# Performance work log

Measured on AMD Instinct MI355X. Metric: run time of the kernel, lower is better.

The kernel has to match this reference:

```python
import jax, jax.numpy as jnp
import numpy as np

# Dims (match init_kwargs / input_specs)
B, N, DIM, HEADS, DHEAD, CHUNK = 1, 2048, 1024, 8, 128, 64
HID = 4 * DHEAD            # MemoryMLP expansion_factor=4.0
DI = HEADS * DHEAD         # dim_inner
EPS = 1e-6
MAX_LR = 1.0               # default_step_transform_max_lr


def rmsnorm(x, w):
    return x * jax.lax.rsqrt(jnp.mean(jnp.square(x), -1, keepdims=True) + EPS) * w


def mem_forward(w0, w1, g, x):
    # ResidualNorm(MemoryMLP): y = RMSNorm(gelu(x@w0)@w1)*g + x
    h = jax.nn.gelu(x @ w0, approximate=False) @ w1
    return rmsnorm(h, g) + x


def setup_inputs() -> dict:
    key = jax.random.key(0)
    ks = jax.random.split(key, 12)
    s = lambda i, shape, sc: jax.random.normal(ks[i], shape, jnp.float32) * sc
    return dict(
        x=s(0, (B, N, DIM), 1.0),
        store_norm_w=jnp.ones((DIM,), jnp.float32),
        ret_norm_w=jnp.ones((DIM,), jnp.float32),
        Wq=s(1, (DIM, DI), DIM ** -0.5),
        Wk=s(2, (DIM, DI), DIM ** -0.5),
        Wv=s(3, (DIM, DI), DIM ** -0.5),
        W_step=s(4, (DIM, HEADS), DIM ** -0.5), b_step=jnp.zeros((HEADS,), jnp.float32),
        W_mom=s(5, (DIM, HEADS), DIM ** -0.5), b_mom=jnp.zeros((HEADS,), jnp.float32),
        W_decay=s(6, (DIM, HEADS), DIM ** -0.5), b_decay=jnp.zeros((HEADS,), jnp.float32),
        gate_W=s(7, (DIM, HEADS), DIM ** -0.5),
        combine_W=s(8, (DI, DIM), DI ** -0.5),
        mem_w0=s(9, (HEADS, DHEAD, HID), DHEAD ** -0.5),
        mem_w1=s(10, (HEADS, HID, DHEAD), HID ** -0.5),
        mem_g=jnp.ones((HEADS, DHEAD), jnp.float32),
    )


def reference(x, store_norm_w, ret_norm_w, Wq, Wk, Wv, W_step, b_step,
              W_mom, b_mom, W_decay, b_decay, gate_W, combine_W,
              mem_w0, mem_w1, mem_g):
    b, n, _ = x.shape
    nc = n // CHUNK
    BH = b * HEADS

    # ---- store path ----
    s = rmsnorm(x, store_norm_w)                                 # b n dim
    lr = jax.nn.sigmoid(s @ W_step + b_step) * MAX_LR            # b n h (per-token adaptive step)
    pooled = s.reshape(b, nc, CHUNK, DIM).mean(2)                # b nc dim (AveragePool chunk rep)
    mom = jax.nn.sigmoid(pooled @ W_mom + b_mom)                 # b nc h
    dec = jax.nn.sigmoid(pooled @ W_decay + b_decay)             # b nc h

    def to_chunks(t):  # b n (h d) -> (b h) nc c d
        return t.reshape(b, nc, CHUNK, HEADS, DHEAD).transpose(0, 3, 1, 2, 4).reshape(BH, nc, CHUNK, DHEAD)

    k = to_chunks(s @ Wk)
    v = to_chunks(s @ Wv)
    lr_c = lr.reshape(b, nc, CHUNK, HEADS).transpose(0, 3, 1, 2).reshape(BH, nc, CHUNK)
    mom_bh = mom.transpose(0, 2, 1).reshape(BH, nc)
    dec_bh = dec.transpose(0, 2, 1).reshape(BH, nc)

    # init fast weights per (b h)  (per_head_learned_parameters=True)
    w0 = jnp.broadcast_to(mem_w0[None], (b, HEADS, DHEAD, HID)).reshape(BH, DHEAD, HID)
    w1 = jnp.broadcast_to(mem_w1[None], (b, HEADS, HID, DHEAD)).reshape(BH, HID, DHEAD)
    g = jnp.broadcast_to(mem_g[None], (b, HEADS, DHEAD)).reshape(BH, DHEAD)

    def chunk_loss(w0_, w1_, g_, kc, vc, lrc):
        pred = mem_forward(w0_, w1_, g_, kc)                     # c d
        return jnp.sum(jnp.mean(jnp.square(pred - vc), -1) * lrc)

    grad_chunk = jax.grad(chunk_loss, argnums=(0, 1, 2))
    # vmap over chunks (same weights per chunk, per-sample grads), then over (b h)
    grads = jax.vmap(jax.vmap(grad_chunk, in_axes=(None, None, None, 0, 0, 0)))(w0, w1, g, k, v, lr_c)
    surprises = tuple(-gr for gr in grads)                       # each (BH, nc, ...)

    def combine(a, c):
        ga, xa = a
        gb, xb = c
        return (ga * gb, gb * xa + xb)

    def lin_scan(gates, xs):
        # y_i = gates_i * y_{i-1} + xs_i over chunk axis (axis=1)
        return jax.lax.associative_scan(combine, (gates, xs), axis=1)

    def expand(gates, ref):
        return gates.reshape(gates.shape + (1,) * (ref.ndim - 2))

    # momentum scan per parameter tensor
    updates = tuple(lin_scan(expand(mom_bh, su), su)[1] for su in surprises)

    # weight update scan: W_i = (1 - decay_i) * W_{i-1} + momentum_i, W_{-1} = init
    per_chunk_weights = []
    for upd, w_init in zip(updates, (w0, w1, g)):
        gates = expand(1.0 - dec_bh, upd)
        cumg, y = lin_scan(gates, upd)
        w_seq = y + cumg * w_init[:, None]                       # (BH, nc, ...)
        # retrieval at chunk i uses weights updated through chunk i-1
        per_chunk_weights.append(jnp.concatenate([w_init[:, None], w_seq[:, :-1]], axis=1))
    w0_c, w1_c, g_c = per_chunk_weights

    # ---- retrieve path ----
    r = rmsnorm(x, ret_norm_w)
    q = to_chunks(r @ Wq)                                        # (BH, nc, c, d)
    pred = jax.vmap(jax.vmap(mem_forward))(w0_c, w1_c, g_c, q)   # (BH, nc, c, d)
    out = pred.reshape(b, HEADS, n, DHEAD)                       # b h n d
    gate = jax.nn.sigmoid(r @ gate_W)                            # b n h (retrieve_gate, heads>1)
    out = out * gate.transpose(0, 2, 1)[..., None]
    out = out.transpose(0, 2, 1, 3).reshape(b, n, DI) @ combine_W
    return out
```

## Files before the change

### kernel.cpp

```cpp
#include <hip/hip_runtime.h>
#include <hip/hip_bf16.h>
#include <math.h>

#define NH   8
#define DHD  128
#define HIDN 512
#define CHK  64
#define NCH  32
#define MB   1048576ull

typedef unsigned short u16;
typedef unsigned int   u32;
typedef short s16x8 __attribute__((ext_vector_type(8)));
typedef float f32x4 __attribute__((ext_vector_type(4)));

#define MFMA(a,b,c) __builtin_amdgcn_mfma_f32_16x16x32_bf16((a),(b),(c),0,0,0)

__device__ __forceinline__ float bf2f(u16 v){ return __uint_as_float(((u32)v) << 16); }
__device__ __forceinline__ u16 f2bf(float f){
  u32 u = __float_as_uint(f);
  u += 0x7fffu + ((u >> 16) & 1u);
  return (u16)(u >> 16);
}
__device__ __forceinline__ u32 pack2(float a, float b){
  return (u32)f2bf(a) | ((u32)f2bf(b) << 16);
}
__device__ __forceinline__ float dot2(u32 a, u32 b){
  return __uint_as_float(a << 16)*__uint_as_float(b << 16)
       + __uint_as_float(a & 0xffff0000u)*__uint_as_float(b & 0xffff0000u);
}
__device__ __forceinline__ float waveRedSum(float v){
  #pragma unroll
  for (int off = 32; off; off >>= 1) v += __shfl_xor(v, off);
  return v;
}
__device__ __forceinline__ void gload16(const void* g, void* l){
  __builtin_amdgcn_global_load_lds(
      (const __attribute__((address_space(1))) u32*)g,
      (__attribute__((address_space(3))) u32*)l, 16, 0, 0);
}
__device__ __forceinline__ int swzb(int row, int colb){ return colb ^ ((row & 7) << 4); }
__device__ __forceinline__ int swza(int row, int colb){
  return colb ^ ((row & 7) << 4) ^ (((row >> 3) & 3) << 5);
}



__global__ __launch_bounds__(256) void k_rmsnorm(const float* __restrict__ x,
    const float* __restrict__ wst, const float* __restrict__ wrt,
    u16* __restrict__ s_bf, u16* __restrict__ r_bf){
  int row = blockIdx.x, t = threadIdx.x;
  float4 v = ((const float4*)(x + (size_t)row*1024))[t];
  float ss = v.x*v.x + v.y*v.y + v.z*v.z + v.w*v.w;
  ss = waveRedSum(ss);
  __shared__ float red[4];
  int wv = t >> 6, ln = t & 63;
  if (ln == 0) red[wv] = ss;
  __syncthreads();
  float rr = rsqrtf((red[0]+red[1]+red[2]+red[3])*(1.f/1024.f) + 1e-6f);
  float4 a = ((const float4*)wst)[t];
  float4 b = ((const float4*)wrt)[t];
  uint2 so = make_uint2(pack2(v.x*rr*a.x, v.y*rr*a.y), pack2(v.z*rr*a.z, v.w*rr*a.w));
  uint2 ro = make_uint2(pack2(v.x*rr*b.x, v.y*rr*b.y), pack2(v.z*rr*b.z, v.w*rr*b.w));
  *(uint2*)(s_bf + (size_t)row*1024 + t*4) = so;
  *(uint2*)(r_bf + (size_t)row*1024 + t*4) = ro;
}

__global__ __launch_bounds__(256) void k_pool(const u16* __restrict__ s_bf, float* __restrict__ pooled){
  int c = blockIdx.x; int d = blockIdx.y*256 + threadIdx.x;
  float acc = 0.f;
  for (int tt = 0; tt < 64; ++tt) acc += bf2f(s_bf[((size_t)c*64+tt)*1024 + d]);
  pooled[(size_t)c*1024 + d] = acc * (1.f/64.f);
}

__global__ __launch_bounds__(256) void k_lrgate(const u16* __restrict__ s_bf, const u16* __restrict__ r_bf,
    const u16* __restrict__ WsgL, const float* __restrict__ bstep,
    float* __restrict__ lrc, float* __restrict__ gate){
  int wv = threadIdx.x >> 6, ln = threadIdx.x & 63;
  int tok = blockIdx.x*4 + wv;
  const u16* sp = s_bf + (size_t)tok*1024 + ln*16;
  const u16* rp = r_bf + (size_t)tok*1024 + ln*16;
  uint4 s0 = *(const uint4*)sp, s1 = *(const uint4*)(sp+8);
  uint4 r0 = *(const uint4*)rp, r1 = *(const uint4*)(rp+8);
  #pragma unroll 4
  for (int o = 0; o < 16; ++o){
    const u16* wp = WsgL + (size_t)o*1024 + ln*16;
    uint4 w0v = *(const uint4*)wp, w1v = *(const uint4*)(wp+8);
    uint4 a0 = (o < 8) ? s0 : r0, a1 = (o < 8) ? s1 : r1;
    float acc = dot2(a0.x,w0v.x)+dot2(a0.y,w0v.y)+dot2(a0.z,w0v.z)+dot2(a0.w,w0v.w)
              + dot2(a1.x,w1v.x)+dot2(a1.y,w1v.y)+dot2(a1.z,w1v.z)+dot2(a1.w,w1v.w);
    acc = waveRedSum(acc);
    if (ln == 0){
      int h = o & 7;
      if (o < 8){
        float v = 1.f/(1.f+expf(-(acc + bstep[h])));
        lrc[((size_t)h*NCH + (tok>>6))*CHK + (tok&63)] = v;
      } else {
        gate[(size_t)tok*8 + h] = 1.f/(1.f+expf(-acc));
      }
    }
  }
}

__global__ __launch_bounds__(64) void k_momdec(const float* __restrict__ pooled,
    const float* __restrict__ Wmom, const float* __restrict__ bmom,
    const float* __restrict__ Wdec, const float* __restrict__ bdec,
    float* __restrict__ momb, float* __restrict__ decb){
  int c = blockIdx.x, ln = threadIdx.x;
  const float* prow = pooled + (size_t)c*1024;
  for (int o = 0; o < 16; ++o){
    int h = o & 7;
    const float* W = (o < 8) ? Wmom : Wdec;
    float acc = 0.f;
    for (int k = ln; k < 1024; k += 64) acc += prow[k]*W[(size_t)k*8+h];
    acc = waveRedSum(acc);
    if (ln == 0){
      float bb = (o < 8) ? bmom[h] : bdec[h];
      float v = 1.f/(1.f+expf(-(acc+bb)));
      if (o < 8) momb[h*NCH + c] = v; else decb[h*NCH + c] = v;
    }
  }
}

__global__ __launch_bounds__(256) void k_trf4(
    const float* __restrict__ A0, const float* __restrict__ A1,
    const float* __restrict__ A2, const float* __restrict__ A3,
    u16* __restrict__ O0, u16* __restrict__ O1, u16* __restrict__ O2, u16* __restrict__ O3){
  __shared__ u16 tile[32][34];
  int z = blockIdx.z;
  const float* in = (z==0)?A0:(z==1)?A1:(z==2)?A2:A3;
  u16* out = (z==0)?O0:(z==1)?O1:(z==2)?O2:O3;
  int c0 = blockIdx.x*32, r0 = blockIdx.y*32;
  int tx = threadIdx.x & 31, ty = threadIdx.x >> 5;
  #pragma unroll
  for (int k = 0; k < 4; ++k) tile[ty+k*8][tx] = f2bf(in[(size_t)(r0+ty+k*8)*1024 + c0+tx]);
  __syncthreads();
  #pragma unroll
  for (int k = 0; k < 4; ++k) out[(size_t)(c0+ty+k*8)*1024 + r0+tx] = tile[tx][ty+k*8];
}

__global__ __launch_bounds__(256) void k_packw(const float* __restrict__ mw0, const float* __restrict__ mw1,
    const float* __restrict__ Wstep, const float* __restrict__ gateW,
    u16* __restrict__ w0L, u16* __restrict__ w1L, u16* __restrict__ w1bL, u16* __restrict__ WsgL){
  int h = blockIdx.z, which = blockIdx.y;
  int i = blockIdx.x*256 + threadIdx.x;
  if (which == 3){
    if (h == 0 && i < 16384){
      int o = i >> 10, k = i & 1023;
      float v = (o < 8) ? Wstep[(size_t)k*8 + o] : gateW[(size_t)k*8 + (o-8)];
      WsgL[i] = f2bf(v);
    }
    return;
// ... 41 lines not shown
        #pragma unroll
        for (int nt = 0; nt < 2; ++nt) acc[mt][nt] = MFMA(xa[mt], yb[nt], acc[mt][nt]);
    }
    __syncthreads();
  }
  #pragma unroll
  for (int mt = 0; mt < 2; ++mt)
    #pragma unroll
    for (int nt = 0; nt < 2; ++nt)
      #pragma unroll
      for (int j = 0; j < 4; ++j){
        int row = bm + wm*32 + mt*16 + lg*4 + j;
        int coln = bn + wn*32 + nt*16 + lr16;
        if (mode == 0) ((float*)Cp)[(size_t)row*1024 + coln] = acc[mt][nt][j];
        else { int cI = row>>6, tok = row&63, h = coln>>7, d = coln&127;
          ((u16*)Cp)[((size_t)(h*32+cI)*64 + tok)*128 + d] = f2bf(acc[mt][nt][j]); }
      }
}

__global__ __launch_bounds__(512) void k_gemm_bf(const u16* __restrict__ A, const u16* __restrict__ BT,
    void* __restrict__ Cp, int mode){ gemm_body(A, BT, Cp, mode); }

__global__ __launch_bounds__(512) void k_gemm3(
    const u16* __restrict__ s_bf, const u16* __restrict__ r_bf,
    const u16* __restrict__ WkT, const u16* __restrict__ WvT, const u16* __restrict__ WqT,
    u16* __restrict__ Kc, u16* __restrict__ Vc, u16* __restrict__ Qc){
  int z = blockIdx.z;
  const u16* A = (z==2) ? r_bf : s_bf;
  const u16* BT = (z==0) ? WkT : (z==1) ? WvT : WqT;
  u16* C = (z==0) ? Kc : (z==1) ? Vc : Qc;
  gemm_body(A, BT, (void*)C, 1);
}

__global__ __launch_bounds__(512, 4) void k_grad(
    const u16* __restrict__ Kc, const u16* __restrict__ Vc, const float* __restrict__ lrc,
    const u16* __restrict__ w0L, const u16* __restrict__ w1L, const u16* __restrict__ w1bL,
    const float* __restrict__ mg,
    u16* __restrict__ SW0, u16* __restrict__ SW1, float* __restrict__ SG, u16* __restrict__ dhg){
  extern __shared__ char sm[];
  char* a_s   = sm;
  char* dhT_s = sm + 65536;
  char* duT_s = a_s;
  char* kcT_s = dhT_s;
  float* scr  = (float*)dhT_s;

  int c = blockIdx.x, bh = blockIdx.y, t = threadIdx.x;
  size_t bc = (size_t)bh*NCH + c;
  int l = t & 63, w = t >> 6, lr16 = l & 15, lg = l >> 4;

  const u16* kc_g = Kc + bc*8192;
  const u16* vc_g = Vc + bc*8192;

  uint2 upr[16];
  const u16* w0Lh = w0L + (size_t)bh*65536;
  #pragma unroll
  for (int tgi = 0; tgi < 4; ++tgi){
    s16x8 xk[4];
    #pragma unroll
    for (int ks = 0; ks < 4; ++ks)
      xk[ks] = *(const s16x8*)(kc_g + (size_t)(tgi*16+lr16)*128 + ks*32 + lg*8);
    #pragma unroll
    for (int n0l = 0; n0l < 4; ++n0l){
      int n0 = w*4 + n0l;
      f32x4 acc = {0.f,0.f,0.f,0.f};
      const u16* yb = w0Lh + (size_t)n0*2048 + l*8;
      #pragma unroll
      for (int ks = 0; ks < 4; ++ks) acc = MFMA(xk[ks], *(const s16x8*)(yb + ks*512), acc);
      int hid = n0*16 + lr16;
      float upv[4];
      #pragma unroll
      for (int j = 0; j < 4; ++j){
        int tok = tgi*16 + lg*4 + j;
        float u = acc[j];
        float cdf = 0.5f*(1.f + erff(u*0.70710678118654752f));
        upv[j] = cdf + u*0.3989422804014327f*expf(-0.5f*u*u);
        *(u16*)(a_s + tok*1024 + swza(tok, hid*2)) = f2bf(u*cdf);
      }
      upr[tgi*4 + n0l] = make_uint2(pack2(upv[0], upv[1]), pack2(upv[2], upv[3]));
    }
  }
  __syncthreads();

  int tg = w & 3, dhf = w >> 2;
  int tokb = tg*16, tok0 = tokb + lg*4;
  const u16* w1Lh = w1L + (size_t)bh*65536;
  f32x4 hD[4];
  #pragma unroll
  for (int n0l = 0; n0l < 4; ++n0l){
    f32x4 acc = {0.f,0.f,0.f,0.f};
    const u16* yb = w1Lh + (size_t)(dhf*4 + n0l)*8192 + l*8;
    #pragma unroll
    for (int kb = 0; kb < 4; ++kb){
      s16x8 xa[4];
      #pragma unroll
      for (int kk = 0; kk < 4; ++kk){
        int k = kb*4 + kk, row = tokb + lr16;
        xa[kk] = *(const s16x8*)(a_s + row*1024 + swza(row, (k*32+lg*8)*2));
      }
      #pragma unroll
      for (int kk = 0; kk < 4; ++kk) acc = MFMA(xa[kk], *(const s16x8*)(yb + (kb*4+kk)*512), acc);
    }
    hD[n0l] = acc;
  }
  #pragma unroll
  for (int j = 0; j < 4; ++j){
    float s = 0.f;
    #pragma unroll
    for (int n0l = 0; n0l < 4; ++n0l) s += hD[n0l][j]*hD[n0l][j];
    s += __shfl_xor(s,1); s += __shfl_xor(s,2); s += __shfl_xor(s,4); s += __shfl_xor(s,8);
    if (lr16 == 0) scr[dhf*64 + tok0 + j] = s;
  }
  __syncthreads();
  float rv[4], lrv[4], dotp[4];
  #pragma unroll
  for (int j = 0; j < 4; ++j){
    int tok = tok0 + j;
    float tot = scr[tok] + scr[64 + tok];
    rv[j] = rsqrtf(tot*(1.f/128.f) + 1e-6f);
    lrv[j] = lrc[bc*64 + tok];
    dotp[j] = 0.f;
  }
  float dn[4][4];
  #pragma unroll
  for (int n0l = 0; n0l < 4; ++n0l){
    int d = dhf*64 + n0l*16 + lr16;
    float g0 = mg[(size_t)bh*128 + d];
    float dgav = 0.f;
    #pragma unroll
    for (int j = 0; j < 4; ++j){
      int tok = tok0 + j;
      float h = hD[n0l][j];
      float nrm = h*rv[j];
      float kcv = bf2f(kc_g[(size_t)tok*128 + d]);
      float vcv = bf2f(vc_g[(size_t)tok*128 + d]);
      float p = nrm*g0 + kcv;
      float dp = (2.f/128.f)*lrv[j]*(p - vcv);
      dgav += dp*nrm;
      float dnv = dp*g0;
      dn[n0l][j] = dnv;
      dotp[j] += dnv*h;
    }
    dgav += __shfl_xor(dgav,16); dgav += __shfl_xor(dgav,32);
    if (lg == 0) scr[256 + w*64 + n0l*16 + lr16] = dgav;
  }
  #pragma unroll
  for (int j = 0; j < 4; ++j){
    float dd = dotp[j];
    dd += __shfl_xor(dd,1); dd += __shfl_xor(dd,2); dd += __shfl_xor(dd,4); dd += __shfl_xor(dd,8);
    if (lr16 == 0) scr[128 + dhf*64 + tok0 + j] = dd;
  }
  __syncthreads();
  float dotv[4];
  #pragma unroll
  for (int j = 0; j < 4; ++j){
    int tok = tok0 + j;
    dotv[j] = scr[128 + tok] + scr[128 + 64 + tok];
  }
  if (t < 128){
    int dh2 = t >> 6, dl = t & 63;
    float s = scr[256 + (dh2*4+0)*64 + dl] + scr[256 + (dh2*4+1)*64 + dl]
            + scr[256 + (dh2*4+2)*64 + dl] + scr[256 + (dh2*4+3)*64 + dl];
    SG[bc*128 + t] = -s;
  }
  __syncthreads();
  #pragma unroll
  for (int n0l = 0; n0l < 4; ++n0l){
    int d = dhf*64 + n0l*16 + lr16;
    float dhv[4];
    #pragma unroll
    for (int j = 0; j < 4; ++j){
      int tok = tok0 + j;
      float c3 = rv[j]*rv[j]*rv[j]*(1.f/128.f);
      dhv[j] = rv[j]*dn[n0l][j] - c3*dotv[j]*hD[n0l][j];
      dhg[bc*8192 + (size_t)tok*128 + d] = f2bf(dhv[j]);
    }
    *(uint2*)(dhT_s + d*128 + swzb(d, tok0*2)) =
        make_uint2(pack2(dhv[0], dhv[1]), pack2(dhv[2], dhv[3]));
  }
  __syncthreads();

  {
    s16x8 yB[4][2];
    #pragma unroll
    for (int n0l = 0; n0l < 4; ++n0l){
      int hid = w*64 + n0l*16 + lr16;
      #pragma unroll
      for (int ks = 0; ks < 2; ++ks){
        s16x8 v;
        #pragma unroll
        for (int e = 0; e < 8; ++e){ int tok = ks*32 + lg*8 + e;
          v[e] = *(const short*)(a_s + tok*1024 + swza(tok, hid*2)); }
        yB[n0l][ks] = v;
      }
    }
    __syncthreads();
    u16* stg = (u16*)(a_s + w*8192);
    #pragma unroll 1
    for (int half = 0; half < 2; ++half){
      #pragma unroll
      for (int mt4 = 0; mt4 < 4; ++mt4){
        int mt = half*4 + mt4; int row = mt*16 + lr16;
        s16x8 xD0 = *(const s16x8*)(dhT_s + row*128 + swzb(row, (lg*8)*2));
        s16x8 xD1 = *(const s16x8*)(dhT_s + row*128 + swzb(row, (32+lg*8)*2));
        #pragma unroll
        for (int n0l = 0; n0l < 4; ++n0l){
          f32x4 acc = {0.f,0.f,0.f,0.f};
          acc = MFMA(xD0, yB[n0l][0], acc);
          acc = MFMA(xD1, yB[n0l][1], acc);
          int base = mt4*1024 + (n0l>>1)*512 + (((n0l*2)+(lr16>>3))&3)*128 + (lr16&7);
          #pragma unroll
          for (int j = 0; j < 4; ++j)
            stg[base + (lg*4+j)*8] = f2bf(-acc[j]);
        }
      }
      asm volatile("s_waitcnt lgkmcnt(0)" ::: "memory");
      #pragma unroll
      for (int mt4 = 0; mt4 < 4; ++mt4){
        int mt = half*4 + mt4;
        u16* gb = SW1 + bc*65536 + (size_t)(mt*16 + w*2)*512;
        s16x8 o0 = *(const s16x8*)(stg + mt4*1024 + l*16);
        s16x8 o1 = *(const s16x8*)(stg + mt4*1024 + l*16 + 8);
        *(s16x8*)(gb + l*16) = o0;
        *(s16x8*)(gb + l*16 + 8) = o1;
      }
    }
  }
  __syncthreads();

  #pragma unroll
  for (int i = 0; i < 2; ++i){
    int idx = i*512 + t;
    int tok = idx & 63, d0 = (idx >> 6)*8;
    s16x8 kv = *(const s16x8*)(kc_g + (size_t)tok*128 + d0);
    #pragma unroll
    for (int e = 0; e < 8; ++e)
      *(u16*)(kcT_s + (d0+e)*128 + swzb(d0+e, tok*2)) = kv[e];
  }
  {
    const u16* dhb = dhg + bc*8192;
    const u16* w1bh = w1bL + (size_t)bh*65536;
    #pragma unroll 1
    for (int mt = 0; mt < 4; ++mt){
      s16x8 xDh[4];
      #pragma unroll
      for (int ks = 0; ks < 4; ++ks)
        xDh[ks] = *(const s16x8*)(dhb + (size_t)(mt*16+lr16)*128 + ks*32 + lg*8);
      #pragma unroll
      for (int n0l = 0; n0l < 4; ++n0l){
        int hid = w*64 + n0l*16 + lr16;
        const u16* xb = w1bh + (size_t)(w*4 + n0l)*2048 + l*8;
        f32x4 acc = {0.f,0.f,0.f,0.f};
        #pragma unroll
        for (int ks = 0; ks < 4; ++ks) acc = MFMA(xDh[ks], *(const s16x8*)(xb + ks*512), acc);
        int tk0 = mt*16 + lg*4;
        uint2 ur = upr[mt*4 + n0l];
        float u0 = bf2f((u16)(ur.x & 0xffff)), u1 = bf2f((u16)(ur.x >> 16));
        float u2 = bf2f((u16)(ur.y & 0xffff)), u3 = bf2f((u16)(ur.y >> 16));
        *(uint2*)(duT_s + hid*128 + swzb(hid, tk0*2)) =
            make_uint2(pack2(acc[0]*u0, acc[1]*u1), pack2(acc[2]*u2, acc[3]*u3));
      }
    }
  }
  __syncthreads();

  {
    s16x8 yK[8][2];
    #pragma unroll
    for (int n0 = 0; n0 < 8; ++n0){
      int d = n0*16 + lr16;
      #pragma unroll
      for (int ks = 0; ks < 2; ++ks)
        yK[n0][ks] = *(const s16x8*)(kcT_s + d*128 + swzb(d, (ks*32+lg*8)*2));
    }
    #pragma unroll 1
    for (int mi = 0; mi < 4; ++mi){
      int hid = w*64 + mi*16 + lr16;
      s16x8 xU0 = *(const s16x8*)(duT_s + hid*128 + swzb(hid, (lg*8)*2));
      s16x8 xU1 = *(const s16x8*)(duT_s + hid*128 + swzb(hid, (32+lg*8)*2));
      u16* stgw = (u16*)(duT_s + (size_t)(w*64 + mi*16)*128);
      u16* gb = SW0 + bc*65536 + (size_t)(w*4 + mi)*2048;
      #pragma unroll 1
      for (int hh = 0; hh < 2; ++hh){
        #pragma unroll
        for (int n0h = 0; n0h < 4; ++n0h){
          int n0 = hh*4 + n0h;
          f32x4 acc = {0.f,0.f,0.f,0.f};
          acc = MFMA(xU0, yK[n0][0], acc);
          acc = MFMA(xU1, yK[n0][1], acc);
          int base = (n0h>>1)*512 + (((n0*2)+(lr16>>3))&3)*128 + (lr16&7);
          #pragma unroll
          for (int j = 0; j < 4; ++j)
            stgw[base + (lg*4+j)*8] = f2bf(-acc[j]);
        }
        asm volatile("s_waitcnt lgkmcnt(0)" ::: "memory");
        s16x8 o0 = *(const s16x8*)(stgw + l*16);
        s16x8 o1 = *(const s16x8*)(stgw + l*16 + 8);
        *(s16x8*)(gb + hh*1024 + l*16) = o0;
        *(s16x8*)(gb + hh*1024 + l*16 + 8) = o1;
      }
    }
  }
}

__global__ __launch_bounds__(256) void k_scan(
    const u16* __restrict__ w0L, const u16* __restrict__ w1L, const float* __restrict__ mg,
    const u16* __restrict__ SW0, const u16* __restrict__ SW1, const float* __restrict__ SG,
    const float* __restrict__ momb, const float* __restrict__ decb,
    u16* __restrict__ W0C, u16* __restrict__ W1C, float* __restrict__ GC){
  int bh = blockIdx.y;
  int e = blockIdx.x*256 + threadIdx.x;
  const float* momp = momb + bh*NCH;
  const float* decp = decb + bh*NCH;
  float m = 0.f, Wv;
  if (e < 65536){
    Wv = bf2f(w0L[(size_t)bh*65536 + e]);
    const u16* su = SW0 + (size_t)bh*NCH*65536 + e;
    u16* outp = W0C + (size_t)bh*NCH*65536 + e;
    for (int c = 0; c < NCH; ++c){
      outp[(size_t)c*65536] = f2bf(Wv);
      m = momp[c]*m + bf2f(su[(size_t)c*65536]);
      Wv = (1.f - decp[c])*Wv + m;
    }
  } else if (e < 131072){
    int e2 = e - 65536;
    Wv = bf2f(w1L[(size_t)bh*65536 + e2]);
    const u16* su = SW1 + (size_t)bh*NCH*65536 + e2;
    u16* outp = W1C + (size_t)bh*NCH*65536 + e2;
    for (int c = 0; c < NCH; ++c){
      outp[(size_t)c*65536] = f2bf(Wv);
      m = momp[c]*m + bf2f(su[(size_t)c*65536]);
      Wv = (1.f - decp[c])*Wv + m;
    }
  } else if (e < 131200){
    int e3 = e - 131072;
    Wv = mg[(size_t)bh*128 + e3];
    const float* su = SG + (size_t)bh*NCH*128 + e3;
    float* outp = GC + (size_t)bh*NCH*128 + e3;
    for (int c = 0; c < NCH; ++c){
      outp[(size_t)c*128] = Wv;
      m = momp[c]*m + su[(size_t)c*128];
      Wv = (1.f - decp[c])*Wv + m;
    }
  }
}

__global__ __launch_bounds__(512) void k_retr(
    const u16* __restrict__ Qc, const u16* __restrict__ W0C, const u16* __restrict__ W1C,
    const float* __restrict__ GC, const float* __restrict__ gate, u16* __restrict__ OH){
  extern __shared__ char sm[];
  char* a_s = sm;
  float* scr = (float*)(sm + 65536);
  int c = blockIdx.x, bh = blockIdx.y, t = threadIdx.x;
  size_t bc = (size_t)bh*NCH + c;
  int l = t & 63, w = t >> 6, lr16 = l & 15, lg = l >> 4;
  int tg = w & 3, dhf = w >> 2;
  const u16* q_g = Qc + bc*8192;

  s16x8 xq[4];
  #pragma unroll
  for (int k = 0; k < 4; ++k)
    xq[k] = *(const s16x8*)(q_g + (size_t)(tg*16+lr16)*128 + k*32 + lg*8);
  const u16* w0c = W0C + bc*65536;
  for (int n0h = 0; n0h < 16; ++n0h){
    int n0 = dhf*16 + n0h;
    f32x4 acc = {0.f,0.f,0.f,0.f};
    const u16* yb = w0c + (size_t)n0*2048 + l*8;
    #pragma unroll
    for (int k = 0; k < 4; ++k) acc = MFMA(xq[k], *(const s16x8*)(yb + k*512), acc);
    int hid = n0*16 + lr16;
    #pragma unroll
    for (int j = 0; j < 4; ++j){
      int tok = tg*16 + lg*4 + j;
      float u = acc[j];
      float av = u*0.5f*(1.f + erff(u*0.70710678118654752f));
      *(u16*)(a_s + tok*1024 + swza(tok, hid*2)) = f2bf(av);
    }
  }
  __syncthreads();
  s16x8 xa[16];
  #pragma unroll
  for (int k = 0; k < 16; ++k){ int row = tg*16 + lr16;
    xa[k] = *(const s16x8*)(a_s + row*1024 + swza(row, (k*32+lg*8)*2)); }
  const u16* w1c = W1C + bc*65536;
  f32x4 hD[4];
  #pragma unroll
  for (int n0l = 0; n0l < 4; ++n0l){
    f32x4 acc = {0.f,0.f,0.f,0.f};
    const u16* yb = w1c + (size_t)(dhf*4 + n0l)*8192 + l*8;
    #pragma unroll
    for (int k = 0; k < 16; ++k) acc = MFMA(xa[k], *(const s16x8*)(yb + k*512), acc);
    hD[n0l] = acc;
  }
  #pragma unroll
  for (int j = 0; j < 4; ++j){
    float s = 0.f;
    #pragma unroll
    for (int n0l = 0; n0l < 4; ++n0l) s += hD[n0l][j]*hD[n0l][j];
    s += __shfl_xor(s,1); s += __shfl_xor(s,2); s += __shfl_xor(s,4); s += __shfl_xor(s,8);
    if (lr16 == 0) scr[dhf*64 + tg*16 + lg*4 + j] = s;
  }
  __syncthreads();
  float rv[4], gtv[4];
  #pragma unroll
  for (int j = 0; j < 4; ++j){
    int tok = tg*16 + lg*4 + j;
    rv[j] = rsqrtf((scr[tok] + scr[64 + tok])*(1.f/128.f) + 1e-6f);
    gtv[j] = gate[(size_t)(c*64 + tok)*8 + bh];
  }
  #pragma unroll
  for (int n0l = 0; n0l < 4; ++n0l){
    int d = dhf*64 + n0l*16 + lr16;
    float g0 = GC[bc*128 + d];
    #pragma unroll
    for (int j = 0; j < 4; ++j){
      int tok = tg*16 + lg*4 + j; int tokg = c*64 + tok;
      float qv = bf2f(q_g[(size_t)tok*128 + d]);
      float p = hD[n0l][j]*rv[j]*g0 + qv;
      OH[(size_t)tokg*1024 + bh*128 + d] = f2bf(p*gtv[j]);
    }
  }
}

extern "C" void kernel_launch(void* const* d_in, const int* in_sizes, int n_in,
                              void* d_out, int out_size, void* d_ws, size_t ws_size,
                              hipStream_t stream) {
  (void)in_sizes; (void)n_in; (void)out_size; (void)ws_size;
  const float* x     = (const float*)d_in[0];
  const float* snw   = (const float*)d_in[1];
  const float* rnw   = (const float*)d_in[2];
  const float* Wq    = (const float*)d_in[3];
  const float* Wk    = (const float*)d_in[4];
  const float* Wv    = (const float*)d_in[5];
  const float* Wstep = (const float*)d_in[6];
  const float* bstep = (const float*)d_in[7];
  const float* Wmom  = (const float*)d_in[8];
  const float* bmom  = (const float*)d_in[9];
  const float* Wdec  = (const float*)d_in[10];
  const float* bdec  = (const float*)d_in[11];
  const float* gateW = (const float*)d_in[12];
  const float* combW = (const float*)d_in[13];
  const float* mw0   = (const float*)d_in[14];
  const float* mw1   = (const float*)d_in[15];
  const float* mg    = (const float*)d_in[16];
  float* out = (float*)d_out;

  char* Wb = (char*)d_ws;
  u16* Qc    = (u16*)(Wb + 0*MB);
  u16* Kc    = (u16*)(Wb + 4*MB);
  u16* Vc    = (u16*)(Wb + 8*MB);
  u16* s_bf  = (u16*)(Wb + 12*MB);
  u16* r_bf  = (u16*)(Wb + 16*MB);
  u16* WqT   = (u16*)(Wb + 20*MB);
  u16* WkT   = (u16*)(Wb + 22*MB);
  u16* WvT   = (u16*)(Wb + 24*MB);
  u16* combT = (u16*)(Wb + 26*MB);
  u16* w0L   = (u16*)(Wb + 28*MB);
  u16* w1L   = (u16*)(Wb + 29*MB);
  u16* w1bL  = (u16*)(Wb + 30*MB);
  u16* OH    = (u16*)(Wb + 31*MB);
  u16* SW0   = (u16*)(Wb + 35*MB);
  u16* SW1   = (u16*)(Wb + 67*MB);
  u16* W0C   = (u16*)(Wb + 99*MB);
  u16* W1C   = (u16*)(Wb + 131*MB);
  float* pooled = (float*)(Wb + 163*MB);
  float* lrc    = (float*)(Wb + 163*MB + 131072);
  float* momb   = (float*)(Wb + 163*MB + 196608);
  float* decb   = (float*)(Wb + 163*MB + 197632);
  float* gate   = (float*)(Wb + 163*MB + 198656);
  float* SG     = (float*)(Wb + 163*MB + 264192);
  float* GC     = (float*)(Wb + 163*MB + 395264);
  u16* WsgL  = (u16*)(Wb + 163*MB + 526336);
  u16* dhg   = (u16*)(Wb + 164*MB);

  hipFuncSetAttribute((const void*)k_grad, hipFuncAttributeMaxDynamicSharedMemorySize, 81920);
  hipFuncSetAttribute((const void*)k_retr, hipFuncAttributeMaxDynamicSharedMemorySize, 66560);

  k_rmsnorm<<<2048, 256, 0, stream>>>(x, snw, rnw, s_bf, r_bf);
  k_pool<<<dim3(32,4), 256, 0, stream>>>(s_bf, pooled);
  k_packw<<<dim3(256,4,8), 256, 0, stream>>>(mw0, mw1, Wstep, gateW, w0L, w1L, w1bL, WsgL);
  k_lrgate<<<512, 256, 0, stream>>>(s_bf, r_bf, WsgL, bstep, lrc, gate);
  k_momdec<<<32, 64, 0, stream>>>(pooled, Wmom, bmom, Wdec, bdec, momb, decb);
  k_trf4<<<dim3(32,32,4), 256, 0, stream>>>(Wq, Wk, Wv, combW, WqT, WkT, WvT, combT);
  k_gemm3<<<dim3(32,8,3), 512, 0, stream>>>(s_bf, r_bf, WkT, WvT, WqT, Kc, Vc, Qc);
  k_grad<<<dim3(32,8), 512, 81920, stream>>>(Kc, Vc, lrc, w0L, w1L, w1bL, mg, SW0, SW1, SG, dhg);
  k_scan<<<dim3(513,8), 256, 0, stream>>>(w0L, w1L, mg, SW0, SW1, SG, momb, decb, W0C, W1C, GC);
  k_retr<<<dim3(32,8), 512, 66560, stream>>>(Qc, W0C, W1C, GC, gate, OH);
  k_gemm_bf<<<dim3(32,8), 512, 0, stream>>>(OH, combT, (void*)out, 0);
}
```

Before: 259.7 us.

## Double threads in grad/retrieve kernels, keep dh and up' in LDS, tanh GELU, fuse small kernels

The gradient and retrieval kernels now run 1024 threads per block, so each wave handles half as much work. The gradient kernel keeps the GELU derivative and dh in LDS (160KB dynamic) instead of registers and a global dh buffer. Exact erf GELU is replaced by a tanh approximation with fast exp, and the lr/gate and momentum/decay kernels are merged into one launch. The aim is more parallelism per chunk and less launch and global traffic, at the cost of GELU accuracy and high LDS use that allows only one block per CU.

```diff
diff --git a/kernel.cpp b/kernel.cpp
--- a/kernel.cpp
+++ b/kernel.cpp
@@ -33,6 +33,15 @@
   #pragma unroll
   for (int off = 32; off; off >>= 1) v += __shfl_xor(v, off);
   return v;
+}
+__device__ __forceinline__ float gelu_v(float u, float& t){
+  float g = 0.7978845608f*(u + 0.044715f*u*u*u);
+  float e = __expf(2.f*g);
+  t = 1.f - __fdividef(2.f, e + 1.f);
+  return 0.5f*u*(1.f + t);
+}
+__device__ __forceinline__ float gelu_d(float u, float t){
+  return 0.5f*(1.f + t) + 0.5f*u*(1.f - t*t)*0.7978845608f*(1.f + 0.134145f*u*u);
 }
 __device__ __forceinline__ void gload16(const void* g, void* l){
   __builtin_amdgcn_global_load_lds(
@@ -73,51 +82,54 @@
   pooled[(size_t)c*1024 + d] = acc * (1.f/64.f);
 }
 
-__global__ __launch_bounds__(256) void k_lrgate(const u16* __restrict__ s_bf, const u16* __restrict__ r_bf,
+__global__ __launch_bounds__(256) void k_lrmd(const u16* __restrict__ s_bf, const u16* __restrict__ r_bf,
     const u16* __restrict__ WsgL, const float* __restrict__ bstep,
-    float* __restrict__ lrc, float* __restrict__ gate){
-  int wv = threadIdx.x >> 6, ln = threadIdx.x & 63;
-  int tok = blockIdx.x*4 + wv;
-  const u16* sp = s_bf + (size_t)tok*1024 + ln*16;
-  const u16* rp = r_bf + (size_t)tok*1024 + ln*16;
-  uint4 s0 = *(const uint4*)sp, s1 = *(const uint4*)(sp+8);
-  uint4 r0 = *(const uint4*)rp, r1 = *(const uint4*)(rp+8);
-  #pragma unroll 4
-  for (int o = 0; o < 16; ++o){
-    const u16* wp = WsgL + (size_t)o*1024 + ln*16;
-    uint4 w0v = *(const uint4*)wp, w1v = *(const uint4*)(wp+8);
-    uint4 a0 = (o < 8) ? s0 : r0, a1 = (o < 8) ? s1 : r1;
-    float acc = dot2(a0.x,w0v.x)+dot2(a0.y,w0v.y)+dot2(a0.z,w0v.z)+dot2(a0.w,w0v.w)
-              + dot2(a1.x,w1v.x)+dot2(a1.y,w1v.y)+dot2(a1.z,w1v.z)+dot2(a1.w,w1v.w);
-    acc = waveRedSum(acc);
-    if (ln == 0){
-      int h = o & 7;
-      if (o < 8){
-        float v = 1.f/(1.f+expf(-(acc + bstep[h])));
-        lrc[((size_t)h*NCH + (tok>>6))*CHK + (tok&63)] = v;
-      } else {
-        gate[(size_t)tok*8 + h] = 1.f/(1.f+expf(-acc));
-      }
-    }
-  }
-}
-
-__global__ __launch_bounds__(64) void k_momdec(const float* __restrict__ pooled,
+    const float* __restrict__ pooled,
     const float* __restrict__ Wmom, const float* __restrict__ bmom,
     const float* __restrict__ Wdec, const float* __restrict__ bdec,
+    float* __restrict__ lrc, float* __restrict__ gate,
     float* __restrict__ momb, float* __restrict__ decb){
-  int c = blockIdx.x, ln = threadIdx.x;
-  const float* prow = pooled + (size_t)c*1024;
-  for (int o = 0; o < 16; ++o){
-    int h = o & 7;
-    const float* W = (o < 8) ? Wmom : Wdec;
-    float acc = 0.f;
-    for (int k = ln; k < 1024; k += 64) acc += prow[k]*W[(size_t)k*8+h];
-    acc = waveRedSum(acc);
-    if (ln == 0){
-      float bb = (o < 8) ? bmom[h] : bdec[h];
-      float v = 1.f/(1.f+expf(-(acc+bb)));
-      if (o < 8) momb[h*NCH + c] = v; else decb[h*NCH + c] = v;
+  int bx = blockIdx.x;
+  if (bx < 512){
+    int wv = threadIdx.x >> 6, ln = threadIdx.x & 63;
+    int tok = bx*4 + wv;
+    const u16* sp = s_bf + (size_t)tok*1024 + ln*16;
+    const u16* rp = r_bf + (size_t)tok*1024 + ln*16;
+    uint4 s0 = *(const uint4*)sp, s1 = *(const uint4*)(sp+8);
+    uint4 r0 = *(const uint4*)rp, r1 = *(const uint4*)(rp+8);
+    #pragma unroll 4
+    for (int o = 0; o < 16; ++o){
+      const u16* wp = WsgL + (size_t)o*1024 + ln*16;
+      uint4 w0v = *(const uint4*)wp, w1v = *(const uint4*)(wp+8);
+      uint4 a0 = (o < 8) ? s0 : r0, a1 = (o < 8) ? s1 : r1;
+      float acc = dot2(a0.x,w0v.x)+dot2(a0.y,w0v.y)+dot2(a0.z,w0v.z)+dot2(a0.w,w0v.w)
+                + dot2(a1.x,w1v.x)+dot2(a1.y,w1v.y)+dot2(a1.z,w1v.z)+dot2(a1.w,w1v.w);
+      acc = waveRedSum(acc);
+      if (ln == 0){
+        int h = o & 7;
+        if (o < 8){
+          float v = 1.f/(1.f+expf(-(acc + bstep[h])));
+          lrc[((size_t)h*NCH + (tok>>6))*CHK + (tok&63)] = v;
+        } else {
+          gate[(size_t)tok*8 + h] = 1.f/(1.f+expf(-acc));
+        }
+      }
+    }
+  } else {
+    if (threadIdx.x >= 64) return;
+    int c = bx - 512, ln = threadIdx.x;
+    const float* prow = pooled + (size_t)c*1024;
+    for (int o = 0; o < 16; ++o){
+      int h = o & 7;
+      const float* W = (o < 8) ? Wmom : Wdec;
+      float acc = 0.f;
+      for (int k = ln; k < 1024; k += 64) acc += prow[k]*W[(size_t)k*8+h];
+      acc = waveRedSum(acc);
+      if (ln == 0){
+        float bb = (o < 8) ? bmom[h] : bdec[h];
+        float v = 1.f/(1.f+expf(-(acc+bb)));
+        if (o < 8) momb[h*NCH + c] = v; else decb[h*NCH + c] = v;
+      }
     }
   }
 }
@@ -225,63 +237,63 @@
   gemm_body(A, BT, (void*)C, 1);
 }
 
-__global__ __launch_bounds__(512, 4) void k_grad(
+__global__ __launch_bounds__(1024, 4) void k_grad(
     const u16* __restrict__ Kc, const u16* __restrict__ Vc, const float* __restrict__ lrc,
     const u16* __restrict__ w0L, const u16* __restrict__ w1L, const u16* __restrict__ w1bL,
     const float* __restrict__ mg,
-    u16* __restrict__ SW0, u16* __restrict__ SW1, float* __restrict__ SG, u16* __restrict__ dhg){
+    u16* __restrict__ SW0, u16* __restrict__ SW1, float* __restrict__ SG){
   extern __shared__ char sm[];
   char* a_s   = sm;
-  char* dhT_s = sm + 65536;
+  char* upT_s = sm + 65536;
+  char* dh_s  = sm + 131072;
+  char* dhT_s = sm + 147456;
   char* duT_s = a_s;
-  char* kcT_s = dhT_s;
-  float* scr  = (float*)dhT_s;
+  char* kcT_s = upT_s;
+  float* scr  = (float*)dh_s;
 
   int c = blockIdx.x, bh = blockIdx.y, t = threadIdx.x;
   size_t bc = (size_t)bh*NCH + c;
   int l = t & 63, w = t >> 6, lr16 = l & 15, lg = l >> 4;
+  int tg = w & 3, hq = w >> 2;
+  int tokb = tg*16, tok0 = tokb + lg*4;
 
   const u16* kc_g = Kc + bc*8192;
   const u16* vc_g = Vc + bc*8192;
 
-  uint2 upr[16];
+  s16x8 xk[4];
+  #pragma unroll
+  for (int ks = 0; ks < 4; ++ks)
+    xk[ks] = *(const s16x8*)(kc_g + (size_t)(tokb+lr16)*128 + ks*32 + lg*8);
   const u16* w0Lh = w0L + (size_t)bh*65536;
   #pragma unroll
-  for (int tgi = 0; tgi < 4; ++tgi){
-    s16x8 xk[4];
-    #pragma unroll
-    for (int ks = 0; ks < 4; ++ks)
-      xk[ks] = *(const s16x8*)(kc_g + (size_t)(tgi*16+lr16)*128 + ks*32 + lg*8);
-    #pragma unroll
-    for (int n0l = 0; n0l < 4; ++n0l){
-      int n0 = w*4 + n0l;
-      f32x4 acc = {0.f,0.f,0.f,0.f};
-      const u16* yb = w0Lh + (size_t)n0*2048 + l*8;
-      #pragma unroll
-      for (int ks = 0; ks < 4; ++ks) acc = MFMA(xk[ks], *(const s16x8*)(yb + ks*512), acc);
-      int hid = n0*16 + lr16;
-      float upv[4];
-      #pragma unroll
-      for (int j = 0; j < 4; ++j){
-        int tok = tgi*16 + lg*4 + j;
-        float u = acc[j];
-        float cdf = 0.5f*(1.f + erff(u*0.70710678118654752f));
-        upv[j] = cdf + u*0.3989422804014327f*expf(-0.5f*u*u);
-        *(u16*)(a_s + tok*1024 + swza(tok, hid*2)) = f2bf(u*cdf);
-      }
-      upr[tgi*4 + n0l] = make_uint2(pack2(upv[0], upv[1]), pack2(upv[2], upv[3]));
-    }
-  }
-  __syncthreads();
-
-  int tg = w & 3, dhf = w >> 2;
-  int tokb = tg*16, tok0 = tokb + lg*4;
+  for (int n0h = 0; n0h < 8; ++n0h){
+    int n0 = hq*8 + n0h;
+    f32x4 acc = {0.f,0.f,0.f,0.f};
+    const u16* yb = w0Lh + (size_t)n0*2048 + l*8;
+    #pragma unroll
+    for (int ks = 0; ks < 4; ++ks) acc = MFMA(xk[ks], *(const s16x8*)(yb + ks*512), acc);
+    int hid = n0*16 + lr16;
+    float upv[4];
+    #pragma unroll
+    for (int j = 0; j < 4; ++j){
+      int tok = tok0 + j;
+      float u = acc[j], tt;
+      float av = gelu_v(u, tt);
+      upv[j] = gelu_d(u, tt);
+      *(u16*)(a_s + tok*1024 + swza(tok, hid*2)) = f2bf(av);
+    }
+    *(uint2*)(upT_s + hid*128 + swzb(hid, tok0*2)) =
+        make_uint2(pack2(upv[0], upv[1]), pack2(upv[2], upv[3]));
+  }
+  __syncthreads();
+
+  int dq = hq;
   const u16* w1Lh = w1L + (size_t)bh*65536;
-  f32x4 hD[4];
-  #pragma unroll
-  for (int n0l = 0; n0l < 4; ++n0l){
+  f32x4 hD[2];
+  #pragma unroll
+  for (int n0l = 0; n0l < 2; ++n0l){
     f32x4 acc = {0.f,0.f,0.f,0.f};
-    const u16* yb = w1Lh + (size_t)(dhf*4 + n0l)*8192 + l*8;
+    const u16* yb = w1Lh + (size_t)(dq*2 + n0l)*8192 + l*8;
     #pragma unroll
     for (int kb = 0; kb < 4; ++kb){
       s16x8 xa[4];
@@ -297,26 +309,24 @@
   }
   #pragma unroll
   for (int j = 0; j < 4; ++j){
-    float s = 0.f;
-    #pragma unroll
-    for (int n0l = 0; n0l < 4; ++n0l) s += hD[n0l][j]*hD[n0l][j];
+    float s = hD[0][j]*hD[0][j] + hD[1][j]*hD[1][j];
     s += __shfl_xor(s,1); s += __shfl_xor(s,2); s += __shfl_xor(s,4); s += __shfl_xor(s,8);
-    if (lr16 == 0) scr[dhf*64 + tok0 + j] = s;
+    if (lr16 == 0) scr[dq*64 + tok0 + j] = s;
   }
   __syncthreads();
   float rv[4], lrv[4], dotp[4];
   #pragma unroll
   for (int j = 0; j < 4; ++j){
     int tok = tok0 + j;
-    float tot = scr[tok] + scr[64 + tok];
+    float tot = scr[tok] + scr[64+tok] + scr[128+tok] + scr[192+tok];
     rv[j] = rsqrtf(tot*(1.f/128.f) + 1e-6f);
     lrv[j] = lrc[bc*64 + tok];
     dotp[j] = 0.f;
   }
-  float dn[4][4];
-  #pragma unroll
-  for (int n0l = 0; n0l < 4; ++n0l){
-    int d = dhf*64 + n0l*16 + lr16;
+  float dn[2][4];
+  #pragma unroll
+  for (int n0l = 0; n0l < 2; ++n0l){
+    int d = dq*32 + n0l*16 + lr16;
     float g0 = mg[(size_t)bh*128 + d];
     float dgav = 0.f;
     #pragma unroll
@@ -334,38 +344,36 @@
       dotp[j] += dnv*h;
     }
     dgav += __shfl_xor(dgav,16); dgav += __shfl_xor(dgav,32);
-    if (lg == 0) scr[256 + w*64 + n0l*16 + lr16] = dgav;
+    if (lg == 0) scr[512 + tg*128 + d] = dgav;
   }
   #pragma unroll
   for (int j = 0; j < 4; ++j){
     float dd = dotp[j];
     dd += __shfl_xor(dd,1); dd += __shfl_xor(dd,2); dd += __shfl_xor(dd,4); dd += __shfl_xor(dd,8);
-    if (lr16 == 0) scr[128 + dhf*64 + tok0 + j] = dd;
+    if (lr16 == 0) scr[256 + dq*64 + tok0 + j] = dd;
   }
   __syncthreads();
   float dotv[4];
   #pragma unroll
   for (int j = 0; j < 4; ++j){
     int tok = tok0 + j;
-    dotv[j] = scr[128 + tok] + scr[128 + 64 + tok];
+    dotv[j] = scr[256+tok] + scr[256+64+tok] + scr[256+128+tok] + scr[256+192+tok];
   }
   if (t < 128){
-    int dh2 = t >> 6, dl = t & 63;
-    float s = scr[256 + (dh2*4+0)*64 + dl] + scr[256 + (dh2*4+1)*64 + dl]
-            + scr[256 + (dh2*4+2)*64 + dl] + scr[256 + (dh2*4+3)*64 + dl];
+    float s = scr[512+t] + scr[512+128+t] + scr[512+256+t] + scr[512+384+t];
     SG[bc*128 + t] = -s;
   }
   __syncthreads();
   #pragma unroll
-  for (int n0l = 0; n0l < 4; ++n0l){
-    int d = dhf*64 + n0l*16 + lr16;
+  for (int n0l = 0; n0l < 2; ++n0l){
+    int d = dq*32 + n0l*16 + lr16;
     float dhv[4];
     #pragma unroll
     for (int j = 0; j < 4; ++j){
       int tok = tok0 + j;
       float c3 = rv[j]*rv[j]*rv[j]*(1.f/128.f);
       dhv[j] = rv[j]*dn[n0l][j] - c3*dotv[j]*hD[n0l][j];
-      dhg[bc*8192 + (size_t)tok*128 + d] = f2bf(dhv[j]);
+      *(u16*)(dh_s + tok*256 + swzb(tok, d*2)) = f2bf(dhv[j]);
     }
     *(uint2*)(dhT_s + d*128 + swzb(d, tok0*2)) =
         make_uint2(pack2(dhv[0], dhv[1]), pack2(dhv[2], dhv[3]));
@@ -373,10 +381,10 @@
   __syncthreads();
 
   {
-    s16x8 yB[4][2];
-    #pragma unroll
-    for (int n0l = 0; n0l < 4; ++n0l){
-      int hid = w*64 + n0l*16 + lr16;
+    s16x8 yB[2][2];
+    #pragma unroll
+    for (int n0l = 0; n0l < 2; ++n0l){
+      int hid = w*32 + n0l*16 + lr16;
       #pragma unroll
       for (int ks = 0; ks < 2; ++ks){
         s16x8 v;
@@ -387,66 +395,52 @@
       }
     }
     __syncthreads();
-    u16* stg = (u16*)(a_s + w*8192);
+    u16* stg = (u16*)(a_s + w*4096);
     #pragma unroll 1
-    for (int half = 0; half < 2; ++half){
-      #pragma unroll
-      for (int mt4 = 0; mt4 < 4; ++mt4){
-        int mt = half*4 + mt4; int row = mt*16 + lr16;
-        s16x8 xD0 = *(const s16x8*)(dhT_s + row*128 + swzb(row, (lg*8)*2));
-        s16x8 xD1 = *(const s16x8*)(dhT_s + row*128 + swzb(row, (32+lg*8)*2));
+    for (int mt = 0; mt < 8; ++mt){
+      int row = mt*16 + lr16;
+      s16x8 xD0 = *(const s16x8*)(dhT_s + row*128 + swzb(row, lg*16));
+      s16x8 xD1 = *(const s16x8*)(dhT_s + row*128 + swzb(row, 64 + lg*16));
+      #pragma unroll
+      for (int n0l = 0; n0l < 2; ++n0l){
+        f32x4 acc = {0.f,0.f,0.f,0.f};
+        acc = MFMA(xD0, yB[n0l][0], acc);
+        acc = MFMA(xD1, yB[n0l][1], acc);
+        int base = ((n0l*2 + (lr16>>3)) & 3)*128 + (lr16 & 7);
         #pragma unroll
-        for (int n0l = 0; n0l < 4; ++n0l){
-          f32x4 acc = {0.f,0.f,0.f,0.f};
-          acc = MFMA(xD0, yB[n0l][0], acc);
-          acc = MFMA(xD1, yB[n0l][1], acc);
-          int base = mt4*1024 + (n0l>>1)*512 + (((n0l*2)+(lr16>>3))&3)*128 + (lr16&7);
-          #pragma unroll
-          for (int j = 0; j < 4; ++j)
-            stg[base + (lg*4+j)*8] = f2bf(-acc[j]);
-        }
+        for (int j = 0; j < 4; ++j)
+          stg[base + (lg*4+j)*8] = f2bf(-acc[j]);
       }
       asm volatile("s_waitcnt lgkmcnt(0)" ::: "memory");
-      #pragma unroll
-      for (int mt4 = 0; mt4 < 4; ++mt4){
-        int mt = half*4 + mt4;
-        u16* gb = SW1 + bc*65536 + (size_t)(mt*16 + w*2)*512;
-        s16x8 o0 = *(const s16x8*)(stg + mt4*1024 + l*16);
-        s16x8 o1 = *(const s16x8*)(stg + mt4*1024 + l*16 + 8);
-        *(s16x8*)(gb + l*16) = o0;
-        *(s16x8*)(gb + l*16 + 8) = o1;
-      }
-    }
-  }
-  __syncthreads();
-
-  #pragma unroll
-  for (int i = 0; i < 2; ++i){
-    int idx = i*512 + t;
-    int tok = idx & 63, d0 = (idx >> 6)*8;
-    s16x8 kv = *(const s16x8*)(kc_g + (size_t)tok*128 + d0);
-    #pragma unroll
-    for (int e = 0; e < 8; ++e)
-      *(u16*)(kcT_s + (d0+e)*128 + swzb(d0+e, tok*2)) = kv[e];
-  }
+      s16x8 o = *(const s16x8*)(stg + l*8);
+      *(s16x8*)(SW1 + bc*65536 + (size_t)(mt*16 + w)*512 + l*8) = o;
+    }
+  }
+  __syncthreads();
+
   {
-    const u16* dhb = dhg + bc*8192;
     const u16* w1bh = w1bL + (size_t)bh*65536;
     #pragma unroll 1
-    for (int mt = 0; mt < 4; ++mt){
-      s16x8 xDh[4];
-      #pragma unroll
-      for (int ks = 0; ks < 4; ++ks)
-        xDh[ks] = *(const s16x8*)(dhb + (size_t)(mt*16+lr16)*128 + ks*32 + lg*8);
-      #pragma unroll
-      for (int n0l = 0; n0l < 4; ++n0l){
-        int hid = w*64 + n0l*16 + lr16;
-        const u16* xb = w1bh + (size_t)(w*4 + n0l)*2048 + l*8;
+    for (int n0l = 0; n0l < 2; ++n0l){
+      int n0 = w*2 + n0l;
+      int hid = n0*16 + lr16;
+      s16x8 yW[4];
+      const u16* xb = w1bh + (size_t)n0*2048 + l*8;
+      #pragma unroll
+      for (int ks = 0; ks < 4; ++ks) yW[ks] = *(const s16x8*)(xb + ks*512);
+      #pragma unroll
+      for (int mt = 0; mt < 4; ++mt){
+        s16x8 xDh[4];
+        #pragma unroll
+        for (int ks = 0; ks < 4; ++ks){
+          int row = mt*16 + lr16;
+          xDh[ks] = *(const s16x8*)(dh_s + row*256 + swzb(row, (ks*32+lg*8)*2));
+        }
         f32x4 acc = {0.f,0.f,0.f,0.f};
         #pragma unroll
-        for (int ks = 0; ks < 4; ++ks) acc = MFMA(xDh[ks], *(const s16x8*)(xb + ks*512), acc);
+        for (int ks = 0; ks < 4; ++ks) acc = MFMA(xDh[ks], yW[ks], acc);
         int tk0 = mt*16 + lg*4;
-        uint2 ur = upr[mt*4 + n0l];
+        uint2 ur = *(const uint2*)(upT_s + hid*128 + swzb(hid, tk0*2));
         float u0 = bf2f((u16)(ur.x & 0xffff)), u1 = bf2f((u16)(ur.x >> 16));
         float u2 = bf2f((u16)(ur.y & 0xffff)), u3 = bf2f((u16)(ur.y >> 16));
         *(uint2*)(duT_s + hid*128 + swzb(hid, tk0*2)) =
@@ -457,30 +451,39 @@
   __syncthreads();
 
   {
+    int tok = t & 63, d0 = (t >> 6)*8;
+    s16x8 kv = *(const s16x8*)(kc_g + (size_t)tok*128 + d0);
+    #pragma unroll
+    for (int e = 0; e < 8; ++e)
+      *(u16*)(kcT_s + (d0+e)*128 + swzb(d0+e, tok*2)) = kv[e];
+  }
+  __syncthreads();
+
+  {
     s16x8 yK[8][2];
     #pragma unroll
-    for (int n0 = 0; n0 < 8; ++n0){
-      int d = n0*16 + lr16;
+    for (int nd = 0; nd < 8; ++nd){
+      int d = nd*16 + lr16;
       #pragma unroll
       for (int ks = 0; ks < 2; ++ks)
-        yK[n0][ks] = *(const s16x8*)(kcT_s + d*128 + swzb(d, (ks*32+lg*8)*2));
+        yK[nd][ks] = *(const s16x8*)(kcT_s + d*128 + swzb(d, (ks*32+lg*8)*2));
     }
     #pragma unroll 1
-    for (int mi = 0; mi < 4; ++mi){
-      int hid = w*64 + mi*16 + lr16;
-      s16x8 xU0 = *(const s16x8*)(duT_s + hid*128 + swzb(hid, (lg*8)*2));
-      s16x8 xU1 = *(const s16x8*)(duT_s + hid*128 + swzb(hid, (32+lg*8)*2));
-      u16* stgw = (u16*)(duT_s + (size_t)(w*64 + mi*16)*128);
-      u16* gb = SW0 + bc*65536 + (size_t)(w*4 + mi)*2048;
+    for (int mi = 0; mi < 2; ++mi){
+      int hid = w*32 + mi*16 + lr16;
+      s16x8 xU0 = *(const s16x8*)(duT_s + hid*128 + swzb(hid, lg*16));
+      s16x8 xU1 = *(const s16x8*)(duT_s + hid*128 + swzb(hid, 64 + lg*16));
+      u16* stgw = (u16*)(duT_s + (size_t)(w*32 + mi*16)*128);
+      u16* gb = SW0 + bc*65536 + (size_t)(w*2 + mi)*2048;
       #pragma unroll 1
-      for (int hh = 0; hh < 2; ++hh){
+      for (int kh = 0; kh < 2; ++kh){
         #pragma unroll
         for (int n0h = 0; n0h < 4; ++n0h){
-          int n0 = hh*4 + n0h;
+          int nd = kh*4 + n0h;
           f32x4 acc = {0.f,0.f,0.f,0.f};
-          acc = MFMA(xU0, yK[n0][0], acc);
-          acc = MFMA(xU1, yK[n0][1], acc);
-          int base = (n0h>>1)*512 + (((n0*2)+(lr16>>3))&3)*128 + (lr16&7);
+          acc = MFMA(xU0, yK[nd][0], acc);
+          acc = MFMA(xU1, yK[nd][1], acc);
+          int base = (n0h>>1)*512 + (((n0h*2)+(lr16>>3))&3)*128 + (lr16&7);
           #pragma unroll
           for (int j = 0; j < 4; ++j)
             stgw[base + (lg*4+j)*8] = f2bf(-acc[j]);
@@ -488,8 +491,8 @@
         asm volatile("s_waitcnt lgkmcnt(0)" ::: "memory");
         s16x8 o0 = *(const s16x8*)(stgw + l*16);
         s16x8 o1 = *(const s16x8*)(stgw + l*16 + 8);
-        *(s16x8*)(gb + hh*1024 + l*16) = o0;
-        *(s16x8*)(gb + hh*1024 + l*16 + 8) = o1;
+        *(s16x8*)(gb + kh*1024 + l*16) = o0;
+        *(s16x8*)(gb + kh*1024 + l*16 + 8) = o1;
       }
     }
   }
@@ -537,7 +540,7 @@
   }
 }
 
-__global__ __launch_bounds__(512) void k_retr(
+__global__ __launch_bounds__(1024, 4) void k_retr(
     const u16* __restrict__ Qc, const u16* __restrict__ W0C, const u16* __restrict__ W1C,
     const float* __restrict__ GC, const float* __restrict__ gate, u16* __restrict__ OH){
   extern __shared__ char sm[];
@@ -546,16 +549,18 @@
   int c = blockIdx.x, bh = blockIdx.y, t = threadIdx.x;
   size_t bc = (size_t)bh*NCH + c;
   int l = t & 63, w = t >> 6, lr16 = l & 15, lg = l >> 4;
-  int tg = w & 3, dhf = w >> 2;
+  int tg = w & 3, hq = w >> 2;
+  int tokb = tg*16, tok0 = tokb + lg*4;
   const u16* q_g = Qc + bc*8192;
 
   s16x8 xq[4];
   #pragma unroll
   for (int k = 0; k < 4; ++k)
-    xq[k] = *(const s16x8*)(q_g + (size_t)(tg*16+lr16)*128 + k*32 + lg*8);
+    xq[k] = *(const s16x8*)(q_g + (size_t)(tokb+lr16)*128 + k*32 + lg*8);
   const u16* w0c = W0C + bc*65536;
-  for (int n0h = 0; n0h < 16; ++n0h){
-    int n0 = dhf*16 + n0h;
+  #pragma unroll
+  for (int n0h = 0; n0h < 8; ++n0h){
+    int n0 = hq*8 + n0h;
     f32x4 acc = {0.f,0.f,0.f,0.f};
     const u16* yb = w0c + (size_t)n0*2048 + l*8;
     #pragma unroll
@@ -563,50 +568,55 @@
     int hid = n0*16 + lr16;
     #pragma unroll
     for (int j = 0; j < 4; ++j){
-      int tok = tg*16 + lg*4 + j;
-      float u = acc[j];
-      float av = u*0.5f*(1.f + erff(u*0.70710678118654752f));
+      int tok = tok0 + j;
+      float u = acc[j], tt;
+      float av = gelu_v(u, tt);
       *(u16*)(a_s + tok*1024 + swza(tok, hid*2)) = f2bf(av);
     }
   }
   __syncthreads();
-  s16x8 xa[16];
-  #pragma unroll
-  for (int k = 0; k < 16; ++k){ int row = tg*16 + lr16;
-    xa[k] = *(const s16x8*)(a_s + row*1024 + swza(row, (k*32+lg*8)*2)); }
+  int dq = hq;
   const u16* w1c = W1C + bc*65536;
-  f32x4 hD[4];
-  #pragma unroll
-  for (int n0l = 0; n0l < 4; ++n0l){
+  f32x4 hD[2];
+  #pragma unroll
+  for (int n0l = 0; n0l < 2; ++n0l){
     f32x4 acc = {0.f,0.f,0.f,0.f};
-    const u16* yb = w1c + (size_t)(dhf*4 + n0l)*8192 + l*8;
-    #pragma unroll
-    for (int k = 0; k < 16; ++k) acc = MFMA(xa[k], *(const s16x8*)(yb + k*512), acc);
+    const u16* yb = w1c + (size_t)(dq*2 + n0l)*8192 + l*8;
+    #pragma unroll
+    for (int kb = 0; kb < 4; ++kb){
+      s16x8 xa[4];
+      #pragma unroll
+      for (int kk = 0; kk < 4; ++kk){
+        int k = kb*4 + kk, row = tokb + lr16;
+        xa[kk] = *(const s16x8*)(a_s + row*1024 + swza(row, (k*32+lg*8)*2));
+      }
+      #pragma unroll
+      for (int kk = 0; kk < 4; ++kk) acc = MFMA(xa[kk], *(const s16x8*)(yb + (kb*4+kk)*512), acc);
+    }
     hD[n0l] = acc;
   }
   #pragma unroll
   for (int j = 0; j < 4; ++j){
-    float s = 0.f;
-    #pragma unroll
-    for (int n0l = 0; n0l < 4; ++n0l) s += hD[n0l][j]*hD[n0l][j];
+    float s = hD[0][j]*hD[0][j] + hD[1][j]*hD[1][j];
     s += __shfl_xor(s,1); s += __shfl_xor(s,2); s += __shfl_xor(s,4); s += __shfl_xor(s,8);
-    if (lr16 == 0) scr[dhf*64 + tg*16 + lg*4 + j] = s;
+    if (lr16 == 0) scr[dq*64 + tok0 + j] = s;
   }
   __syncthreads();
   float rv[4], gtv[4];
   #pragma unroll
   for (int j = 0; j < 4; ++j){
-    int tok = tg*16 + lg*4 + j;
-    rv[j] = rsqrtf((scr[tok] + scr[64 + tok])*(1.f/128.f) + 1e-6f);
+    int tok = tok0 + j;
+    float tot = scr[tok] + scr[64+tok] + scr[128+tok] + scr[192+tok];
+    rv[j] = rsqrtf(tot*(1.f/128.f) + 1e-6f);
     gtv[j] = gate[(size_t)(c*64 + tok)*8 + bh];
   }
   #pragma unroll
-  for (int n0l = 0; n0l < 4; ++n0l){
-    int d = dhf*64 + n0l*16 + lr16;
+  for (int n0l = 0; n0l < 2; ++n0l){
+    int d = dq*32 + n0l*16 + lr16;
     float g0 = GC[bc*128 + d];
     #pragma unroll
     for (int j = 0; j < 4; ++j){
-      int tok = tg*16 + lg*4 + j; int tokg = c*64 + tok;
+      int tok = tok0 + j; int tokg = c*64 + tok;
       float qv = bf2f(q_g[(size_t)tok*128 + d]);
       float p = hD[n0l][j]*rv[j]*g0 + qv;
       OH[(size_t)tokg*1024 + bh*128 + d] = f2bf(p*gtv[j]);
@@ -663,20 +673,19 @@
   float* SG     = (float*)(Wb + 163*MB + 264192);
   float* GC     = (float*)(Wb + 163*MB + 395264);
   u16* WsgL  = (u16*)(Wb + 163*MB + 526336);
-  u16* dhg   = (u16*)(Wb + 164*MB);
-
-  hipFuncSetAttribute((const void*)k_grad, hipFuncAttributeMaxDynamicSharedMemorySize, 81920);
+
+  hipFuncSetAttribute((const void*)k_grad, hipFuncAttributeMaxDynamicSharedMemorySize, 163840);
   hipFuncSetAttribute((const void*)k_retr, hipFuncAttributeMaxDynamicSharedMemorySize, 66560);
 
   k_rmsnorm<<<2048, 256, 0, stream>>>(x, snw, rnw, s_bf, r_bf);
   k_pool<<<dim3(32,4), 256, 0, stream>>>(s_bf, pooled);
   k_packw<<<dim3(256,4,8), 256, 0, stream>>>(mw0, mw1, Wstep, gateW, w0L, w1L, w1bL, WsgL);
-  k_lrgate<<<512, 256, 0, stream>>>(s_bf, r_bf, WsgL, bstep, lrc, gate);
-  k_momdec<<<32, 64, 0, stream>>>(pooled, Wmom, bmom, Wdec, bdec, momb, decb);
+  k_lrmd<<<544, 256, 0, stream>>>(s_bf, r_bf, WsgL, bstep, pooled, Wmom, bmom, Wdec, bdec,
+                                  lrc, gate, momb, decb);
   k_trf4<<<dim3(32,32,4), 256, 0, stream>>>(Wq, Wk, Wv, combW, WqT, WkT, WvT, combT);
   k_gemm3<<<dim3(32,8,3), 512, 0, stream>>>(s_bf, r_bf, WkT, WvT, WqT, Kc, Vc, Qc);
-  k_grad<<<dim3(32,8), 512, 81920, stream>>>(Kc, Vc, lrc, w0L, w1L, w1bL, mg, SW0, SW1, SG, dhg);
+  k_grad<<<dim3(32,8), 1024, 163840, stream>>>(Kc, Vc, lrc, w0L, w1L, w1bL, mg, SW0, SW1, SG);
   k_scan<<<dim3(513,8), 256, 0, stream>>>(w0L, w1L, mg, SW0, SW1, SG, momb, decb, W0C, W1C, GC);
-  k_retr<<<dim3(32,8), 512, 66560, stream>>>(Qc, W0C, W1C, GC, gate, OH);
+  k_retr<<<dim3(32,8), 1024, 66560, stream>>>(Qc, W0C, W1C, GC, gate, OH);
   k_gemm_bf<<<dim3(32,8), 512, 0, stream>>>(OH, combT, (void*)out, 0);
 }
```

Measured after the change: 229.2 us. 11.7% less time.
